# Kernel tuning notes

Hardware: AMD Instinct MI355X
Metric: run time of the kernel (lower is better)

## Reference

```python
import jax, jax.numpy as jnp
import numpy as np

B = 64; IMG = 224; P = 16; CIN = 3
DM = 192; DEPTH = 24; DSTATE = 16; DINNER = 384; DTR = 12; DCONV = 4
N = (IMG // P) ** 2  # 196 tokens


def setup_inputs() -> dict:
    key = jax.random.key(0)
    ks = jax.random.split(key, 10)
    s = 0.02
    img = jax.random.normal(ks[0], (B, CIN, IMG, IMG), jnp.float32)
    patch_w = jax.random.normal(ks[1], (DM, CIN, P, P), jnp.float32) * s
    patch_b = jnp.zeros((DM,), jnp.float32)
    # per-layer Mamba params, stacked along depth
    in_proj_w = jax.random.normal(ks[2], (DEPTH, 2 * DINNER, DM), jnp.float32) * s
    conv_w = jax.random.normal(ks[3], (DEPTH, DINNER, DCONV), jnp.float32) * s
    conv_b = jnp.zeros((DEPTH, DINNER), jnp.float32)
    x_proj_w = jax.random.normal(ks[4], (DEPTH, DTR + 2 * DSTATE, DINNER), jnp.float32) * s
    dt_w = jax.random.normal(ks[5], (DEPTH, DINNER, DTR), jnp.float32) * s
    dt_b = jax.random.normal(ks[6], (DEPTH, DINNER), jnp.float32) * s
    # S4D-real init: A = -[1..d_state]
    A_log = jnp.log(jnp.broadcast_to(jnp.arange(1, DSTATE + 1, dtype=jnp.float32), (DEPTH, DINNER, DSTATE)))
    D_param = jnp.ones((DEPTH, DINNER), jnp.float32)
    out_proj_w = jax.random.normal(ks[7], (DEPTH, DM, DINNER), jnp.float32) * s
    norm_w = jnp.ones((DM,), jnp.float32)
    norm_b = jnp.zeros((DM,), jnp.float32)
    return dict(img=img, patch_w=patch_w, patch_b=patch_b, in_proj_w=in_proj_w,
                conv_w=conv_w, conv_b=conv_b, x_proj_w=x_proj_w, dt_w=dt_w, dt_b=dt_b,
                A_log=A_log, D_param=D_param, out_proj_w=out_proj_w,
                norm_w=norm_w, norm_b=norm_b)


def _mamba(x, p):
    # x: (B, L, DM); one Mamba mixer block (mamba_ssm semantics, no residual)
    in_w, cw, cb, xpw, dtw, dtb, A_log, Dv, outw = p
    Bb, L, _ = x.shape
    xz = jnp.einsum('bld,ed->ble', x, in_w)          # (B,L,2*DINNER)
    xs, z = jnp.split(xz, 2, axis=-1)
    # causal depthwise conv1d, kernel size DCONV
    xpad = jnp.pad(xs, ((0, 0), (DCONV - 1, 0), (0, 0)))
    xc = cb + sum(xpad[:, k:k + L, :] * cw[:, k] for k in range(DCONV))
    xc = jax.nn.silu(xc)
    proj = jnp.einsum('bld,ed->ble', xc, xpw)        # (B,L,DTR+2*DSTATE)
    dt = jax.nn.softplus(jnp.einsum('blr,dr->bld', proj[..., :DTR], dtw) + dtb)  # (B,L,DINNER)
    Bm = proj[..., DTR:DTR + DSTATE]                 # (B,L,DSTATE)
    Cm = proj[..., DTR + DSTATE:]                    # (B,L,DSTATE)
    A = -jnp.exp(A_log)                              # (DINNER,DSTATE)

    def step(h, inp):
        dt_t, B_t, u_t, C_t = inp                    # (B,DINNER),(B,DSTATE),(B,DINNER),(B,DSTATE)
        dA = jnp.exp(dt_t[:, :, None] * A)
        h = h * dA + dt_t[:, :, None] * B_t[:, None, :] * u_t[:, :, None]
        y = jnp.einsum('bds,bs->bd', h, C_t)
        return h, y

    h0 = jnp.zeros((Bb, DINNER, DSTATE), x.dtype)
    _, ys = jax.lax.scan(step, h0, (dt.transpose(1, 0, 2), Bm.transpose(1, 0, 2),
                                    xc.transpose(1, 0, 2), Cm.transpose(1, 0, 2)))
    y = ys.transpose(1, 0, 2) + xc * Dv
    y = y * jax.nn.silu(z)
    return jnp.einsum('bld,od->blo', y, outw)


def _forward(img, patch_w, patch_b, in_proj_w, conv_w, conv_b, x_proj_w, dt_w, dt_b,
             A_log, D_param, out_proj_w, norm_w, norm_b):
    x = jax.lax.conv_general_dilated(img, patch_w, (P, P), 'VALID',
                                     dimension_numbers=('NCHW', 'OIHW', 'NCHW'))
    x = x + patch_b[None, :, None, None]
    x = x.reshape(x.shape[0], DM, N).transpose(0, 2, 1)  # (B,N,DM)

    def layer(c, p):
        return _mamba(c, p), None

    x, _ = jax.lax.scan(layer, x, (in_proj_w, conv_w, conv_b, x_proj_w, dt_w, dt_b,
                                   A_log, D_param, out_proj_w))
    mu = x.mean(-1, keepdims=True)
    var = ((x - mu) ** 2).mean(-1, keepdims=True)
    x = (x - mu) / jnp.sqrt(var + 1e-5) * norm_w + norm_b
    return x.mean(axis=1)  # pooled (B, DM)


def reference(img, patch_w, patch_b, in_proj_w, conv_w, conv_b, x_proj_w, dt_w, dt_b,
              A_log, D_param, out_proj_w, norm_w, norm_b):
    return _forward(img, patch_w, patch_b, in_proj_w, conv_w, conv_b, x_proj_w,
                    dt_w, dt_b, A_log, D_param, out_proj_w, norm_w, norm_b)
```

## Files before the change

kernel.cpp:

```cpp
#include <hip/hip_runtime.h>
#include <hip/hip_bf16.h>
#include <math.h>

#define BB 64
#define IMG 224
#define PP 16
#define CIN 3
#define DM 192
#define DEPTH 24
#define DSTATE 16
#define DINNER 384
#define DTR 12
#define DCONV 4
#define NP 196
#define RTOT (BB * NP)
#define CHUNKS 14
#define LC 14
#define NCMB (2 * DSTATE + DINNER)

typedef short bf16x8 __attribute__((ext_vector_type(8)));
typedef float f32x4 __attribute__((ext_vector_type(4)));

__device__ inline unsigned short f2bf_rne(float f) {
    unsigned u = __float_as_uint(f);
    unsigned r = u + 0x7fffu + ((u >> 16) & 1u);
    return (unsigned short)(r >> 16);
}
__device__ inline float bf2f(unsigned short s) {
    return __uint_as_float(((unsigned)s) << 16);
}

__global__ __launch_bounds__(256) void im2col_pack_kernel(const float* __restrict__ img,
                                                          short* __restrict__ colH) {
    size_t idx = (size_t)blockIdx.x * 256 + threadIdx.x;
    if (idx >= (size_t)RTOT * 768) return;
    int t = (int)(idx % 768);
    size_t r = idx / 768;
    int l = (int)(r % NP);
    int b = (int)(r / NP);
    int ph = l / 14, pw = l % 14;
    int ci = t / 256, rem = t % 256;
    int i = rem / 16, j = rem % 16;
    float v = img[(((size_t)b * CIN + ci) * IMG + ph * 16 + i) * IMG + pw * 16 + j];
    colH[idx] = (short)f2bf_rne(v);
}

__global__ __launch_bounds__(256) void pack_w_kernel(const float* __restrict__ W,
                                                     short* __restrict__ Wh, int NE) {
    int i = blockIdx.x * 256 + threadIdx.x;
    if (i * 4 >= NE) return;
    float4 v = *(const float4*)&W[i * 4];
    short4 h;
    h.x = (short)f2bf_rne(v.x);
    h.y = (short)f2bf_rne(v.y);
    h.z = (short)f2bf_rne(v.z);
    h.w = (short)f2bf_rne(v.w);
    *(short4*)&Wh[i * 4] = h;
}

__global__ __launch_bounds__(256) void wcmb_kernel(const float* __restrict__ xpw,
                                                   const float* __restrict__ dtw,
                                                   short* __restrict__ wCmb) {
    int idx = blockIdx.x * 256 + threadIdx.x;
    if (idx >= DEPTH * NCMB * DINNER) return;
    int layer = idx / (NCMB * DINNER);
    int rem = idx % (NCMB * DINNER);
    int n = rem / DINNER;
    int k = rem % DINNER;
    const float* xp = xpw + (size_t)layer * 44 * DINNER;
    float v;
    if (n < 32) {
        v = xp[(DTR + n) * DINNER + k];
    } else {
        int d = n - 32;
        const float* w = dtw + ((size_t)layer * DINNER + d) * DTR;
        v = 0.f;
#pragma unroll
        for (int j = 0; j < DTR; j++) v += w[j] * xp[j * DINNER + k];
    }
    wCmb[idx] = (short)f2bf_rne(v);
}

template<int BM, int BN>
__global__ __launch_bounds__(256) void gemm_pk_kernel(const short* __restrict__ Ah,
                                                      const short* __restrict__ Bh,
                                                      float* __restrict__ C,
                                                      short* __restrict__ CBf,
                                                      const float* __restrict__ bias,
                                                      int M, int N, int K, int Kc) {
    constexpr int BK = 32;
    constexpr int LDSS = BK + 8;
    constexpr int WR = BM / 64;
    constexpr int WC = 4 / WR;
    constexpr int NJ = BN / WC / 16;
    constexpr int A8 = BM / 64;
    constexpr int B8 = BN / 64;
    __shared__ short As[2][BM * LDSS];
    __shared__ short Bs[2][BN * LDSS];

    const int tid = threadIdx.x;
    const int lane = tid & 63;
    const int wid = tid >> 6;
    const int wr = wid / WC, wc = wid % WC;
    const int row0 = blockIdx.y * BM, col0 = blockIdx.x * BN;
    const int kbase = blockIdx.z * Kc;
    const bf16x8 ZV = {0, 0, 0, 0, 0, 0, 0, 0};

    bf16x8 aPh[A8], bPh[B8];
    f32x4 acc[4][NJ] = {};

    auto loadG = [&](int k0) {
#pragma unroll
        for (int i = 0; i < A8; i++) {
            int lin = tid + i * 256;
            int r = lin >> 2, cg = (lin & 3) * 8;
            aPh[i] = *(const bf16x8*)&Ah[(size_t)(row0 + r) * K + k0 + cg];
        }
#pragma unroll
        for (int i = 0; i < B8; i++) {
            int lin = tid + i * 256;
            int r = lin >> 2, cg = (lin & 3) * 8;
            int n = col0 + r;
            bPh[i] = (n < N) ? *(const bf16x8*)&Bh[(size_t)n * K + k0 + cg] : ZV;
        }
    };
    auto storeLDS = [&](int p) {
#pragma unroll
        for (int i = 0; i < A8; i++) {
            int lin = tid + i * 256;
            int r = lin >> 2, cg = (lin & 3) * 8;
            *(bf16x8*)&As[p][r * LDSS + cg] = aPh[i];
        }
#pragma unroll
        for (int i = 0; i < B8; i++) {
            int lin = tid + i * 256;
            int r = lin >> 2, cg = (lin & 3) * 8;
            *(bf16x8*)&Bs[p][r * LDSS + cg] = bPh[i];
        }
    };
    auto compute = [&](int p) {
        const int fr = lane & 15;
        const int kg = (lane >> 4) * 8;
        bf16x8 aH[4], bH[NJ];
#pragma unroll
        for (int i = 0; i < 4; i++)
            aH[i] = *(const bf16x8*)&As[p][(wr * 64 + i * 16 + fr) * LDSS + kg];
#pragma unroll
        for (int j = 0; j < NJ; j++)
            bH[j] = *(const bf16x8*)&Bs[p][(wc * (BN / WC) + j * 16 + fr) * LDSS + kg];
#pragma unroll
        for (int i = 0; i < 4; i++)
#pragma unroll
            for (int j = 0; j < NJ; j++)
                acc[i][j] = __builtin_amdgcn_mfma_f32_16x16x32_bf16(aH[i], bH[j], acc[i][j], 0, 0, 0);
    };

    loadG(kbase);
    storeLDS(0);
    __syncthreads();
    int p = 0;
    for (int k0 = kbase + BK;; k0 += BK) {
        const bool has_next = (k0 < kbase + Kc);
        if (has_next) loadG(k0);
        compute(p);
        if (!has_next) break;
        storeLDS(p ^ 1);
        __syncthreads();
        p ^= 1;
    }

    const bool direct = (gridDim.z == 1);
    float* Cout = C + (size_t)blockIdx.z * M * N;
    const int crow = (lane >> 4) * 4;
    const int ccol = lane & 15;
#pragma unroll
    for (int i = 0; i < 4; i++)
#pragma unroll
        for (int j = 0; j < NJ; j++) {
            int gn = col0 + wc * (BN / WC) + j * 16 + ccol;
            if (gn >= N) continue;
            int gm0 = row0 + wr * 64 + i * 16 + crow;
            float bv = (direct && bias) ? bias[gn] : 0.f;
            if (direct && CBf) {
#pragma unroll
                for (int reg = 0; reg < 4; reg++)
                    CBf[(size_t)(gm0 + reg) * N + gn] = (short)f2bf_rne(acc[i][j][reg] + bv);
            } else {
#pragma unroll
                for (int reg = 0; reg < 4; reg++)
                    Cout[(size_t)(gm0 + reg) * N + gn] = acc[i][j][reg] + bv;
            }
        }
}

__global__ __launch_bounds__(256) void gemm_xproj_kernel(const short* __restrict__ Ah,
                                                         const short* __restrict__ Bh,
                                                         float* __restrict__ projBC,
                                                         short* __restrict__ dtB,
                                                         const float* __restrict__ dtb,
                                                         int M, int K) {
    constexpr int BM = 64, BN = 64, BK = 32;
    constexpr int LDSS = BK + 8;
    constexpr int N = NCMB;
    __shared__ short As[2][BM * LDSS];
    __shared__ short Bs[2][BN * LDSS];

    const int tid = threadIdx.x;
    const int lane = tid & 63;
    const int wc = tid >> 6;
    const int row0 = blockIdx.y * BM, col0 = blockIdx.x * BN;
    const bf16x8 ZV = {0, 0, 0, 0, 0, 0, 0, 0};

    bf16x8 aPh, bPh;
    f32x4 acc[4] = {};

    auto loadG = [&](int k0) {
        int r = tid >> 2, cg = (tid & 3) * 8;
        aPh = *(const bf16x8*)&Ah[(size_t)(row0 + r) * K + k0 + cg];
        int n = col0 + r;
        bPh = (n < N) ? *(const bf16x8*)&Bh[(size_t)n * K + k0 + cg] : ZV;
    };
    auto storeLDS = [&](int p) {
        int r = tid >> 2, cg = (tid & 3) * 8;
        *(bf16x8*)&As[p][r * LDSS + cg] = aPh;
        *(bf16x8*)&Bs[p][r * LDSS + cg] = bPh;
    };
    auto compute = [&](int p) {
        const int fr = lane & 15;
        const int kg = (lane >> 4) * 8;
        bf16x8 aH[4], bH;
#pragma unroll
        for (int i = 0; i < 4; i++)
            aH[i] = *(const bf16x8*)&As[p][(i * 16 + fr) * LDSS + kg];
        bH = *(const bf16x8*)&Bs[p][(wc * 16 + fr) * LDSS + kg];
#pragma unroll
        for (int i = 0; i < 4; i++)
            acc[i] = __builtin_amdgcn_mfma_f32_16x16x32_bf16(aH[i], bH, acc[i], 0, 0, 0);
    };

    loadG(0);
    storeLDS(0);
    __syncthreads();
    int p = 0;
    for (int k0 = BK;; k0 += BK) {
        const bool has_next = (k0 < K);
        if (has_next) loadG(k0);
        compute(p);
        if (!has_next) break;
        storeLDS(p ^ 1);
        __syncthreads();
        p ^= 1;
    }

    const int crow = (lane >> 4) * 4;
    const int ccol = lane & 15;
#pragma unroll
    for (int i = 0; i < 4; i++) {
        int gn = col0 + wc * 16 + ccol;
        if (gn >= NCMB) continue;
        int gm0 = row0 + i * 16 + crow;
        if (gn < 32) {
#pragma unroll
            for (int reg = 0; reg < 4; reg++)
                projBC[(size_t)(gm0 + reg) * 32 + gn] = acc[i][reg];
        } else {
            int d = gn - 32;
            float bv = dtb[d];
#pragma unroll
            for (int reg = 0; reg < 4; reg++) {
                float v = acc[i][reg] + bv;
                v = (v > 20.f) ? v : __logf(1.f + __expf(v));
                dtB[(size_t)(gm0 + reg) * DINNER + d] = (short)f2bf_rne(v);
            }
        }
    }
}

__global__ __launch_bounds__(256) void reduce_kernel(const float* __restrict__ parts,
                                                     short* __restrict__ outH,
                                                     const float* __restrict__ bias,
                                                     long MN, int N, int SK) {
    long i = (long)blockIdx.x * 256 + threadIdx.x;
    if (i * 4 >= MN) return;
    float4 acc = *(const float4*)&parts[i * 4];
    for (int z = 1; z < SK; z++) {
        float4 v = *(const float4*)&parts[(size_t)z * MN + i * 4];
        acc.x += v.x; acc.y += v.y; acc.z += v.z; acc.w += v.w;
    }
    if (bias) {
        int col = (int)((i * 4) % N);
        float4 bv = *(const float4*)&bias[col];
        acc.x += bv.x; acc.y += bv.y; acc.z += bv.z; acc.w += bv.w;
    }
    short4 h;
    h.x = (short)f2bf_rne(acc.x);
    h.y = (short)f2bf_rne(acc.y);
    h.z = (short)f2bf_rne(acc.z);
    h.w = (short)f2bf_rne(acc.w);
    *(short4*)&outH[i * 4] = h;
}

__global__ __launch_bounds__(256) void conv_silu_kernel(const short* __restrict__ xzBf,
                                                        const float* __restrict__ cw,
                                                        const float* __restrict__ cb,
                                                        short* __restrict__ xcH) {
    size_t idx = (size_t)blockIdx.x * 256 + threadIdx.x;
    if (idx >= (size_t)RTOT * (DINNER / 4)) return;
    int e0 = (int)(idx % (DINNER / 4)) * 4;
    size_t r = idx / (DINNER / 4);
    int l = (int)(r % NP);
    size_t b = r / NP;
    float acc[4];
    {
        float4 cbv = *(const float4*)&cb[e0];
        acc[0] = cbv.x; acc[1] = cbv.y; acc[2] = cbv.z; acc[3] = cbv.w;
    }
    float4 wv[4];
#pragma unroll
    for (int j = 0; j < 4; j++) wv[j] = *(const float4*)&cw[(e0 + j) * DCONV];
#pragma unroll
    for (int k = 0; k < DCONV; k++) {
        int ls = l + k - (DCONV - 1);
        if (ls >= 0) {
            short4 xv = *(const short4*)&xzBf[(b * NP + ls) * 768 + e0];
            acc[0] += bf2f((unsigned short)xv.x) * (&wv[0].x)[k];
            acc[1] += bf2f((unsigned short)xv.y) * (&wv[1].x)[k];
            acc[2] += bf2f((unsigned short)xv.z) * (&wv[2].x)[k];
            acc[3] += bf2f((unsigned short)xv.w) * (&wv[3].x)[k];
        }
    }
    short4 o;
#pragma unroll
    for (int j = 0; j < 4; j++) {
        float v = acc[j] / (1.f + __expf(-acc[j]));
        (&o.x)[j] = (short)f2bf_rne(v);
    }
    *(short4*)&xcH[r * DINNER + e0] = o;
}

__global__ __launch_bounds__(128) void scanA_kernel(const short* __restrict__ xcB,
                                                    const float* __restrict__ projBC,
                                                    const short* __restrict__ dtB,
                                                    const float* __restrict__ A_log,
                                                    float* __restrict__ hEnd,
                                                    float* __restrict__ prodDA) {
    int d = blockIdx.x * 128 + threadIdx.x;
    int c = blockIdx.y, b = blockIdx.z;
    float a[DSTATE], h[DSTATE];
#pragma unroll
    for (int s = 0; s < DSTATE; s++) {
        a[s] = -expf(A_log[(size_t)d * DSTATE + s]);
        h[s] = 0.f;
    }
    const float a0 = a[0];
    bool chain = true;
#pragma unroll
    for (int s = 1; s < DSTATE; s++)
        chain = chain && (fabsf(a[s] - (float)(s + 1) * a0) <= 1e-4f * fabsf(a[s]));
    float sdt = 0.f;
    size_t rbase = (size_t)b * NP + (size_t)c * LC;
    if (chain) {
        for (int l = 0; l < LC; l++) {
            size_t r = rbase + l;
            float dtv = bf2f((unsigned short)dtB[r * DINNER + d]);
            float du = dtv * bf2f((unsigned short)xcB[r * DINNER + d]);
            const float* pb = projBC + r * 32;
            float Bv[DSTATE];
            *(float4*)&Bv[0]  = *(const float4*)&pb[0];
            *(float4*)&Bv[4]  = *(const float4*)&pb[4];
            *(float4*)&Bv[8]  = *(const float4*)&pb[8];
            *(float4*)&Bv[12] = *(const float4*)&pb[12];
            float q = __expf(dtv * a0);
            float dA = q;
            h[0] = h[0] * dA + du * Bv[0];
#pragma unroll
            for (int s = 1; s < DSTATE; s++) {
                dA *= q;
                h[s] = h[s] * dA + du * Bv[s];
            }
            sdt += dtv;
        }
    } else {
        for (int l = 0; l < LC; l++) {
            size_t r = rbase + l;
            float dtv = bf2f((unsigned short)dtB[r * DINNER + d]);
            float du = dtv * bf2f((unsigned short)xcB[r * DINNER + d]);
            const float* pb = projBC + r * 32;
            float Bv[DSTATE];
            *(float4*)&Bv[0]  = *(const float4*)&pb[0];
            *(float4*)&Bv[4]  = *(const float4*)&pb[4];
            *(float4*)&Bv[8]  = *(const float4*)&pb[8];
            *(float4*)&Bv[12] = *(const float4*)&pb[12];
#pragma unroll
            for (int s = 0; s < DSTATE; s++) {
                float dA = __expf(dtv * a[s]);
                h[s] = h[s] * dA + du * Bv[s];
            }
            sdt += dtv;
        }
    }
    float* he = hEnd   + (((size_t)b * CHUNKS + c) * DINNER + d) * DSTATE;
    float* pd = prodDA + (((size_t)b * CHUNKS + c) * DINNER + d) * DSTATE;
#pragma unroll
    for (int g = 0; g < 4; g++)
        *(float4*)&he[g * 4] = *(float4*)&h[g * 4];
    float pv[DSTATE];
#pragma unroll
    for (int s = 0; s < DSTATE; s++) pv[s] = __expf(a[s] * sdt);
#pragma unroll
    for (int g = 0; g < 4; g++)
        *(float4*)&pd[g * 4] = *(float4*)&pv[g * 4];
}

__global__ __launch_bounds__(256) void scanB_kernel(const float* __restrict__ hEnd,
                                                    float* __restrict__ prodDA) {
    int idx = blockIdx.x * 256 + threadIdx.x;
    if (idx >= BB * DINNER * DSTATE) return;
    int b = idx / (DINNER * DSTATE);
    int rem = idx % (DINNER * DSTATE);
    float run = 0.f;
    for (int c = 0; c < CHUNKS; c++) {
        size_t off = ((size_t)b * CHUNKS + c) * (DINNER * DSTATE) + rem;
        float p = prodDA[off];
        float e = hEnd[off];
        prodDA[off] = run;
        run = run * p + e;
    }
}

__global__ __launch_bounds__(128) void scanC_kernel(const short* __restrict__ xcB,
                                                    const float* __restrict__ projBC,
                                                    const short* __restrict__ dtB,
                                                    const float* __restrict__ hInit,
                                                    const float* __restrict__ A_log,
                                                    const float* __restrict__ Dv,
                                                    const short* __restrict__ xzBf,
                                                    short* __restrict__ yh) {
    int d = blockIdx.x * 128 + threadIdx.x;
    int c = blockIdx.y, b = blockIdx.z;
    float a[DSTATE], h[DSTATE];
#pragma unroll
    for (int s = 0; s < DSTATE; s++)
        a[s] = -expf(A_log[(size_t)d * DSTATE + s]);
    const float a0 = a[0];
    bool chain = true;
#pragma unroll
    for (int s = 1; s < DSTATE; s++)
        chain = chain && (fabsf(a[s] - (float)(s + 1) * a0) <= 1e-4f * fabsf(a[s]));
    const float* hi = hInit + (((size_t)b * CHUNKS + c) * DINNER + d) * DSTATE;
#pragma unroll
    for (int g = 0; g < 4; g++)
        *(float4*)&h[g * 4] = *(const float4*)&hi[g * 4];
    float Dd = Dv[d];
    size_t rbase = (size_t)b * NP + (size_t)c * LC;
    if (chain) {
        for (int l = 0; l < LC; l++) {
            size_t r = rbase + l;
            float dtv = bf2f((unsigned short)dtB[r * DINNER + d]);
            float u = bf2f((unsigned short)xcB[r * DINNER + d]);
            float du = dtv * u;
            const float* pb = projBC + r * 32;
            float Bv[DSTATE], Cv[DSTATE];
            *(float4*)&Bv[0]  = *(const float4*)&pb[0];
            *(float4*)&Bv[4]  = *(const float4*)&pb[4];
            *(float4*)&Bv[8]  = *(const float4*)&pb[8];
            *(float4*)&Bv[12] = *(const float4*)&pb[12];
            *(float4*)&Cv[0]  = *(const float4*)&pb[16];
            *(float4*)&Cv[4]  = *(const float4*)&pb[20];
            *(float4*)&Cv[8]  = *(const float4*)&pb[24];
            *(float4*)&Cv[12] = *(const float4*)&pb[28];
            float q = __expf(dtv * a0);
            float dA = q;
            h[0] = h[0] * dA + du * Bv[0];
            float y = h[0] * Cv[0];
#pragma unroll
            for (int s = 1; s < DSTATE; s++) {
                dA *= q;
                h[s] = h[s] * dA + du * Bv[s];
                y = fmaf(h[s], Cv[s], y);
            }
            float z = bf2f((unsigned short)xzBf[r * 768 + DINNER + d]);
            float val = (y + u * Dd) * (z / (1.f + __expf(-z)));
            yh[r * DINNER + d] = (short)f2bf_rne(val);
        }
    } else {
        for (int l = 0; l < LC; l++) {
            size_t r = rbase + l;
            float dtv = bf2f((unsigned short)dtB[r * DINNER + d]);
            float u = bf2f((unsigned short)xcB[r * DINNER + d]);
            float du = dtv * u;
            const float* pb = projBC + r * 32;
            float Bv[DSTATE], Cv[DSTATE];
            *(float4*)&Bv[0]  = *(const float4*)&pb[0];
            *(float4*)&Bv[4]  = *(const float4*)&pb[4];
            *(float4*)&Bv[8]  = *(const float4*)&pb[8];
            *(float4*)&Bv[12] = *(const float4*)&pb[12];
            *(float4*)&Cv[0]  = *(const float4*)&pb[16];
            *(float4*)&Cv[4]  = *(const float4*)&pb[20];
            *(float4*)&Cv[8]  = *(const float4*)&pb[24];
            *(float4*)&Cv[12] = *(const float4*)&pb[28];
            float y = 0.f;
#pragma unroll
            for (int s = 0; s < DSTATE; s++) {
                float dA = __expf(dtv * a[s]);
                h[s] = h[s] * dA + du * Bv[s];
                y = fmaf(h[s], Cv[s], y);
            }
            float z = bf2f((unsigned short)xzBf[r * 768 + DINNER + d]);
            float val = (y + u * Dd) * (z / (1.f + __expf(-z)));
            yh[r * DINNER + d] = (short)f2bf_rne(val);
        }
    }
}

__global__ __launch_bounds__(256) void ln_stats_kernel(const short* __restrict__ xh,
                                                       float* __restrict__ stats) {
    int r = blockIdx.x * 4 + (threadIdx.x >> 6);
    int lane = threadIdx.x & 63;
    if (r >= RTOT) return;
    float s = 0.f, ss = 0.f;
    for (int c = lane; c < DM; c += 64) {
        float v = bf2f((unsigned short)xh[(size_t)r * DM + c]);
        s += v;
        ss += v * v;
    }
#pragma unroll
    for (int o = 32; o > 0; o >>= 1) {
        s += __shfl_down(s, o);
        ss += __shfl_down(ss, o);
    }
    if (lane == 0) {
        float mu = s / (float)DM;
        float var = ss / (float)DM - mu * mu;
        stats[r * 2] = mu;
        stats[r * 2 + 1] = rsqrtf(var + 1e-5f);
    }
}

__global__ __launch_bounds__(256) void ln_mean_kernel(const short* __restrict__ xh,
                                                      const float* __restrict__ stats,
                                                      const float* __restrict__ nw,
                                                      const float* __restrict__ nb,
                                                      float* __restrict__ out) {
    int idx = blockIdx.x * 256 + threadIdx.x;
    if (idx >= BB * DM) return;
    int c = idx % DM;
    int b = idx / DM;
    float acc = 0.f;
    for (int l = 0; l < NP; l++) {
        size_t r = (size_t)b * NP + l;
        float v = bf2f((unsigned short)xh[r * DM + c]);
        acc += (v - stats[r * 2]) * stats[r * 2 + 1];
    }
    out[idx] = acc * (1.f / (float)NP) * nw[c] + nb[c];
}

extern "C" void kernel_launch(void* const* d_in, const int* in_sizes, int n_in,
                              void* d_out, int out_size, void* d_ws, size_t ws_size,
                              hipStream_t stream) {
    const float* img     = (const float*)d_in[0];
    const float* patch_w = (const float*)d_in[1];
    const float* patch_b = (const float*)d_in[2];
    const float* in_w    = (const float*)d_in[3];
    const float* conv_w  = (const float*)d_in[4];
    const float* conv_b  = (const float*)d_in[5];
    const float* xpw     = (const float*)d_in[6];
    const float* dtw     = (const float*)d_in[7];
    const float* dtb     = (const float*)d_in[8];
    const float* A_log   = (const float*)d_in[9];
    const float* Dv      = (const float*)d_in[10];
    const float* outw    = (const float*)d_in[11];
    const float* norm_w  = (const float*)d_in[12];
    const float* norm_b  = (const float*)d_in[13];
    float* out = (float*)d_out;

    float* ws = (float*)d_ws;
    const size_t R = RTOT;
    const size_t SCN = (size_t)BB * CHUNKS * DINNER * DSTATE;

    float* xA      = ws;
    float* xB      = xA + R * DM / 2;
    float* xzB     = xB + R * DM / 2;
    float* xcB     = xzB + R * 768 / 2;
    float* dtBf    = xcB + R * DINNER / 2;
    float* projBC  = dtBf + R * DINNER / 2;
    float* scratch = projBC + R * 32;
    float* wAll    = scratch + 2 * SCN;
    float* stats   = wAll + 4644864;

    short* wPatch = (short*)wAll;
    short* wIn    = wPatch + (size_t)DM * 768;
    short* wOut   = wIn + (size_t)DEPTH * 2 * DINNER * DM;
    short* wCmb   = wOut + (size_t)DEPTH * DM * DINNER;

    short* y2h = (short*)scratch;

    pack_w_kernel<<<dim3((DM * 768 / 4 + 255) / 256), 256, 0, stream>>>(
        patch_w, wPatch, DM * 768);
    pack_w_kernel<<<dim3((DEPTH * 2 * DINNER * DM / 4 + 255) / 256), 256, 0, stream>>>(
        in_w, wIn, DEPTH * 2 * DINNER * DM);
    pack_w_kernel<<<dim3((DEPTH * DM * DINNER / 4 + 255) / 256), 256, 0, stream>>>(
        outw, wOut, DEPTH * DM * DINNER);
    wcmb_kernel<<<dim3((DEPTH * NCMB * DINNER + 255) / 256), 256, 0, stream>>>(
        xpw, dtw, wCmb);

    {
        short* colH = (short*)xzB;
        size_t n = R * 768;
        im2col_pack_kernel<<<dim3((unsigned)((n + 255) / 256)), 256, 0, stream>>>(img, colH);
        gemm_pk_kernel<64, 64><<<dim3(3, RTOT / 64, 4), 256, 0, stream>>>(
            colH, wPatch, scratch, nullptr, nullptr, RTOT, DM, 768, 192);
        long MN = (long)RTOT * DM;
        reduce_kernel<<<dim3((unsigned)((MN / 4 + 255) / 256)), 256, 0, stream>>>(
            scratch, (short*)xA, patch_b, MN, DM, 4);
    }

    float* xin = xA;
    float* xout = xB;
    for (int layer = 0; layer < DEPTH; layer++) {
        const float* conv_wl = conv_w + (size_t)layer * DINNER * DCONV;
        const float* conv_bl = conv_b + (size_t)layer * DINNER;
        const float* dtb_l   = dtb + (size_t)layer * DINNER;
        const float* Alog_l  = A_log + (size_t)layer * DINNER * DSTATE;
        const float* Dv_l    = Dv + (size_t)layer * DINNER;
        short* wIn_l  = wIn + (size_t)layer * 2 * DINNER * DM;
        short* wOut_l = wOut + (size_t)layer * DM * DINNER;
        short* wCmb_l = wCmb + (size_t)layer * NCMB * DINNER;

        short* xinH = (short*)xin;
        short* xoutH = (short*)xout;
        short* xzH = (short*)xzB;
        short* xcH = (short*)xcB;
        short* dtH = (short*)dtBf;

        gemm_pk_kernel<64, 128><<<dim3(768 / 128, RTOT / 64, 1), 256, 0, stream>>>(
            xinH, wIn_l, nullptr, xzH, nullptr, RTOT, 2 * DINNER, DM, DM);
        {
            size_t n = R * (DINNER / 4);
            conv_silu_kernel<<<dim3((unsigned)((n + 255) / 256)), 256, 0, stream>>>(
                xzH, conv_wl, conv_bl, xcH);
        }
        gemm_xproj_kernel<<<dim3(7, RTOT / 64), 256, 0, stream>>>(
            xcH, wCmb_l, projBC, dtH, dtb_l, RTOT, DINNER);
        scanA_kernel<<<dim3(3, CHUNKS, BB), 128, 0, stream>>>(
            xcH, projBC, dtH, Alog_l, scratch, scratch + SCN);
        scanB_kernel<<<dim3((BB * DINNER * DSTATE + 255) / 256), 256, 0, stream>>>(
            scratch, scratch + SCN);
        scanC_kernel<<<dim3(3, CHUNKS, BB), 128, 0, stream>>>(
            xcH, projBC, dtH, scratch + SCN, Alog_l, Dv_l, xzH, y2h);
        gemm_pk_kernel<64, 64><<<dim3(DM / 64, RTOT / 64, 1), 256, 0, stream>>>(
            y2h, wOut_l, nullptr, xoutH, nullptr, RTOT, DM, DINNER, DINNER);

        float* t = xin; xin = xout; xout = t;
    }

    short* xfH = (short*)xin;
    ln_stats_kernel<<<dim3(RTOT / 4), 256, 0, stream>>>(xfH, stats);
    ln_mean_kernel<<<dim3((BB * DM + 255) / 256), 256, 0, stream>>>(
        xfH, stats, norm_w, norm_b, out);
}
```

Baseline: 2.930 ms.

## Fold out_proj of each layer into next layer's in_proj weight

There is no residual or norm between Mamba layers, so the out_proj of layer l and the in_proj of layer l+1 are consecutive linear maps. A new prep kernel multiplies them into a single 768x384 bf16 weight per layer boundary, and one GEMM from y2h straight to xz replaces the two GEMMs. This removes a launch and the write and read of the 192-wide intermediate per layer. In exchange it costs more MACs per row, adds an fp32 precompute kernel run on every call, and changes bf16 rounding because the product is rounded once instead of twice.

New measurement: 3.060 ms. 4.4% more time.

```diff
diff --git a/kernel.cpp b/kernel.cpp
--- a/kernel.cpp
+++ b/kernel.cpp
@@ -79,6 +79,34 @@
         for (int j = 0; j < DTR; j++) v += w[j] * xp[j * DINNER + k];
     }
     wCmb[idx] = (short)f2bf_rne(v);
+}
+
+__global__ __launch_bounds__(256) void wcross_kernel(const float* __restrict__ in_w,
+                                                     const float* __restrict__ outw,
+                                                     short* __restrict__ wCross) {
+    int idx = blockIdx.x * 256 + threadIdx.x;
+    if (idx >= (DEPTH - 1) * 768 * (DINNER / 4)) return;
+    int lid = idx / (768 * (DINNER / 4));
+    int rem = idx % (768 * (DINNER / 4));
+    int n = rem / (DINNER / 4);
+    int k4 = (rem % (DINNER / 4)) * 4;
+    const float* A = in_w + ((size_t)(lid + 1)) * 768 * DM + (size_t)n * DM;
+    const float* Bp = outw + (size_t)lid * DM * DINNER + k4;
+    float4 acc = make_float4(0.f, 0.f, 0.f, 0.f);
+    for (int m = 0; m < DM; m++) {
+        float w = A[m];
+        float4 o = *(const float4*)&Bp[(size_t)m * DINNER];
+        acc.x = fmaf(w, o.x, acc.x);
+        acc.y = fmaf(w, o.y, acc.y);
+        acc.z = fmaf(w, o.z, acc.z);
+        acc.w = fmaf(w, o.w, acc.w);
+    }
+    short4 h;
+    h.x = (short)f2bf_rne(acc.x);
+    h.y = (short)f2bf_rne(acc.y);
+    h.z = (short)f2bf_rne(acc.z);
+    h.w = (short)f2bf_rne(acc.w);
+    *(short4*)&wCross[(size_t)lid * 768 * DINNER + (size_t)n * DINNER + k4] = h;
 }
 
 template<int BM, int BN>
@@ -586,12 +614,14 @@
     float* projBC  = dtBf + R * DINNER / 2;
     float* scratch = projBC + R * 32;
     float* wAll    = scratch + 2 * SCN;
-    float* stats   = wAll + 4644864;
+    float* wCrossF = wAll + 4644864;
+    float* stats   = wCrossF + 3391488;
 
     short* wPatch = (short*)wAll;
     short* wIn    = wPatch + (size_t)DM * 768;
     short* wOut   = wIn + (size_t)DEPTH * 2 * DINNER * DM;
     short* wCmb   = wOut + (size_t)DEPTH * DM * DINNER;
+    short* wCross = (short*)wCrossF;
 
     short* y2h = (short*)scratch;
 
@@ -603,6 +633,8 @@
         outw, wOut, DEPTH * DM * DINNER);
     wcmb_kernel<<<dim3((DEPTH * NCMB * DINNER + 255) / 256), 256, 0, stream>>>(
         xpw, dtw, wCmb);
+    wcross_kernel<<<dim3(((DEPTH - 1) * 768 * (DINNER / 4) + 255) / 256), 256, 0, stream>>>(
+        in_w, outw, wCross);
 
     {
         short* colH = (short*)xzB;
@@ -615,26 +647,21 @@
             scratch, (short*)xA, patch_b, MN, DM, 4);
     }
 
-    float* xin = xA;
-    float* xout = xB;
+    short* xzH = (short*)xzB;
+    short* xcH = (short*)xcB;
+    short* dtH = (short*)dtBf;
+
+    gemm_pk_kernel<64, 128><<<dim3(768 / 128, RTOT / 64, 1), 256, 0, stream>>>(
+        (short*)xA, wIn, nullptr, xzH, nullptr, RTOT, 2 * DINNER, DM, DM);
+
     for (int layer = 0; layer < DEPTH; layer++) {
         const float* conv_wl = conv_w + (size_t)layer * DINNER * DCONV;
         const float* conv_bl = conv_b + (size_t)layer * DINNER;
         const float* dtb_l   = dtb + (size_t)layer * DINNER;
         const float* Alog_l  = A_log + (size_t)layer * DINNER * DSTATE;
         const float* Dv_l    = Dv + (size_t)layer * DINNER;
-        short* wIn_l  = wIn + (size_t)layer * 2 * DINNER * DM;
-        short* wOut_l = wOut + (size_t)layer * DM * DINNER;
         short* wCmb_l = wCmb + (size_t)layer * NCMB * DINNER;
 
-        short* xinH = (short*)xin;
-        short* xoutH = (short*)xout;
-        short* xzH = (short*)xzB;
-        short* xcH = (short*)xcB;
-        short* dtH = (short*)dtBf;
-
-        gemm_pk_kernel<64, 128><<<dim3(768 / 128, RTOT / 64, 1), 256, 0, stream>>>(
-            xinH, wIn_l, nullptr, xzH, nullptr, RTOT, 2 * DINNER, DM, DM);
         {
             size_t n = R * (DINNER / 4);
             conv_silu_kernel<<<dim3((unsigned)((n + 255) / 256)), 256, 0, stream>>>(
@@ -648,13 +675,18 @@
             scratch, scratch + SCN);
         scanC_kernel<<<dim3(3, CHUNKS, BB), 128, 0, stream>>>(
             xcH, projBC, dtH, scratch + SCN, Alog_l, Dv_l, xzH, y2h);
-        gemm_pk_kernel<64, 64><<<dim3(DM / 64, RTOT / 64, 1), 256, 0, stream>>>(
-            y2h, wOut_l, nullptr, xoutH, nullptr, RTOT, DM, DINNER, DINNER);
-
-        float* t = xin; xin = xout; xout = t;
-    }
-
-    short* xfH = (short*)xin;
+        if (layer < DEPTH - 1) {
+            short* wX = wCross + (size_t)layer * 768 * DINNER;
+            gemm_pk_kernel<64, 128><<<dim3(768 / 128, RTOT / 64, 1), 256, 0, stream>>>(
+                y2h, wX, nullptr, xzH, nullptr, RTOT, 2 * DINNER, DINNER, DINNER);
+        } else {
+            short* wOut_l = wOut + (size_t)layer * DM * DINNER;
+            gemm_pk_kernel<64, 64><<<dim3(DM / 64, RTOT / 64, 1), 256, 0, stream>>>(
+                y2h, wOut_l, nullptr, (short*)xB, nullptr, RTOT, DM, DINNER, DINNER);
+        }
+    }
+
+    short* xfH = (short*)xB;
     ln_stats_kernel<<<dim3(RTOT / 4), 256, 0, stream>>>(xfH, stats);
     ln_mean_kernel<<<dim3((BB * DM + 255) / 256), 256, 0, stream>>>(
         xfH, stats, norm_w, norm_b, out);
```
